# Performance work log

Hardware: AMD Instinct MI355X
Metric: run time of the kernel (lower is better)

Reference implementation:

```python
import jax, jax.numpy as jnp
import numpy as np

WS = 8                       # window size (square)
N = WS * WS                  # tokens per window
RES_H, RES_W = 32, 32        # input_resolution
DIM = 512
NUM_HEADS = 16
HEAD_DIM = DIM // NUM_HEADS
SCALE = HEAD_DIM ** -0.5
TABLE = 2 * WS - 1           # size of a_p/b_p/a_r/b_r tables
B_ = 1024                    # num_windows * batch


def _rel_coords():
    c = np.arange(WS)
    coords = np.stack(np.meshgrid(c, c, indexing='ij'))          # (2, WS, WS)
    cf = coords.reshape(2, -1)                                   # (2, N)
    rel = cf[:, :, None] - cf[:, None, :]                        # (2, N, N), values in [-(WS-1), WS-1]
    return rel[0], rel[1]                                        # radius (dh), azimuth (dw)

RADIUS_NP, AZIMUTH_NP = _rel_coords()
# torch indexes the (2*WS-1)-row tables with negative indices -> python wrap: -k maps to TABLE-k
IDX_R = jnp.asarray(RADIUS_NP % TABLE)
IDX_AZ = jnp.asarray(AZIMUTH_NP % TABLE)
RADIUS = jnp.asarray(RADIUS_NP, dtype=jnp.float32)               # (N, N)
AZIMUTH = jnp.asarray(AZIMUTH_NP, dtype=jnp.float32)             # (N, N)


def setup_inputs() -> dict:
    key = jax.random.key(0)
    ks = jax.random.split(key, 10)
    return {
        'x': jax.random.normal(ks[0], (B_, N, DIM), dtype=jnp.float32),
        'theta_max': jnp.ones((), dtype=jnp.float32) * 1.5708,   # ~pi/2 field-of-view half-angle
        'qkv_w': jax.random.normal(ks[1], (3 * DIM, DIM), dtype=jnp.float32) * 0.02,
        'qkv_b': jnp.zeros((3 * DIM,), dtype=jnp.float32),
        'proj_w': jax.random.normal(ks[2], (DIM, DIM), dtype=jnp.float32) * 0.02,
        'proj_b': jnp.zeros((DIM,), dtype=jnp.float32),
        'a_p': jax.random.normal(ks[3], (TABLE, NUM_HEADS), dtype=jnp.float32) * 0.02,
        'b_p': jax.random.normal(ks[4], (TABLE, NUM_HEADS), dtype=jnp.float32) * 0.02,
        'a_r': jax.random.normal(ks[5], (TABLE, NUM_HEADS), dtype=jnp.float32) * 0.02,
        'b_r': jax.random.normal(ks[6], (TABLE, NUM_HEADS), dtype=jnp.float32) * 0.02,
    }


def _trig_bias(table_a, table_b, idx, angle):
    # table_[ab]: (TABLE, H); idx: (N, N) int; angle: (N, N) float (possibly traced)
    a = table_a[idx]                                              # (N, N, H)
    b = table_b[idx]
    ang = angle[:, :, None]                                       # (N, N, 1)
    bias = a * jnp.cos(ang) + b * jnp.sin(ang)                    # (N, N, H)
    return jnp.transpose(bias, (2, 0, 1))                         # (H, N, N)


def reference(x, theta_max, qkv_w, qkv_b, proj_w, proj_b, a_p, b_p, a_r, b_r):
    Bw, n, c = x.shape
    qkv = x @ qkv_w.T + qkv_b                                     # (B_, N, 3*DIM)
    qkv = qkv.reshape(Bw, n, 3, NUM_HEADS, HEAD_DIM)
    qkv = jnp.transpose(qkv, (2, 0, 3, 1, 4))                     # (3, B_, H, N, hd)
    q, k, v = qkv[0] * SCALE, qkv[1], qkv[2]

    attn = jnp.einsum('bhid,bhjd->bhij', q, k)                    # (B_, H, N, N)

    az_angle = AZIMUTH * (2.0 * np.pi / RES_W)                    # (N, N)
    A_phi = _trig_bias(a_p, b_p, IDX_AZ, az_angle)                # (H, N, N)
    r_angle = RADIUS * (theta_max / RES_H)                        # (N, N), traced via theta_max
    A_theta = _trig_bias(a_r, b_r, IDX_R, r_angle)                # (H, N, N)

    attn = attn + A_phi[None] + A_theta[None]
    attn = jax.nn.softmax(attn, axis=-1)

    out = jnp.einsum('bhij,bhjd->bhid', attn, v)                  # (B_, H, N, hd)
    out = jnp.transpose(out, (0, 2, 1, 3)).reshape(Bw, n, c)      # (B_, N, DIM)
    out = out @ proj_w.T + proj_b
    return out
```

## Files before the change

kernel.cpp:

```cpp
#include <hip/hip_runtime.h>
#include <hip/hip_bf16.h>


typedef __bf16 bf16_t;
typedef bf16_t bf16x4 __attribute__((ext_vector_type(4)));
typedef bf16_t bf16x8 __attribute__((ext_vector_type(8)));
typedef float  f32x4  __attribute__((ext_vector_type(4)));

#define NWIN   1024
#define NTOK   64
#define DIM    512
#define NHEADS 16
#define HD     32
#define MTOT   (NWIN*NTOK)
#define QKVN   (3*DIM)
#define SCLG2E 0.25503494f

__device__ __forceinline__ void async_copy16(const void* g, void* lds_generic) {
    __builtin_amdgcn_global_load_lds(
        (__attribute__((address_space(1))) unsigned int*)(unsigned long long)g,
        (__attribute__((address_space(3))) unsigned int*)(unsigned int)(unsigned long long)lds_generic,
        16, 0, 0);
}

__global__ void cvt_f32_bf16(const float* __restrict__ in, bf16_t* __restrict__ out, int n8) {
    int i = blockIdx.x * blockDim.x + threadIdx.x;
    if (i >= n8) return;
    const float4* p = (const float4*)in;
    float4 a = p[2*i], b = p[2*i+1];
    bf16x8 o;
    o[0]=(bf16_t)a.x; o[1]=(bf16_t)a.y; o[2]=(bf16_t)a.z; o[3]=(bf16_t)a.w;
    o[4]=(bf16_t)b.x; o[5]=(bf16_t)b.y; o[6]=(bf16_t)b.z; o[7]=(bf16_t)b.w;
    ((bf16x8*)out)[i] = o;
}

__global__ void bias_kernel(const float* __restrict__ ap, const float* __restrict__ bp,
                            const float* __restrict__ ar, const float* __restrict__ br,
                            const float* __restrict__ theta_max, float* __restrict__ bias) {
    int idx = blockIdx.x * 256 + threadIdx.x;
    int h  = idx >> 12;
    int ij = idx & 4095;
    int i = ij >> 6, j = ij & 63;
    int ri = i >> 3, ci = i & 7, rj = j >> 3, cj = j & 7;
    int rad = ri - rj, az = ci - cj;
    int idx_r  = rad < 0 ? rad + 15 : rad;
    int idx_az = az  < 0 ? az  + 15 : az;
    float azang = (float)az * 0.19634954084936207f;
    float rang  = (float)rad * (theta_max[0] * (1.0f/32.0f));
    float v = ap[idx_az*NHEADS + h] * cosf(azang) + bp[idx_az*NHEADS + h] * sinf(azang)
            + ar[idx_r *NHEADS + h] * cosf(rang)  + br[idx_r *NHEADS + h] * sinf(rang);
    bias[idx] = v * 1.4426950408889634f;
}

template<int OUT_BF16>
__global__ __launch_bounds__(256, 2)
void gemm_bt(const bf16_t* __restrict__ A, const bf16_t* __restrict__ Bt,
             const float* __restrict__ bias, void* __restrict__ C,
             int M, int N, int K, int ntiles) {
    __shared__ bf16_t sA[128*64];
    __shared__ bf16_t sB[128*64];

    int bid = blockIdx.x;
    int bm = bid / ntiles, bn = bid % ntiles;
    int tid = threadIdx.x;
    int w = tid >> 6, lane = tid & 63;
    int quad = lane >> 4, l16 = lane & 15;
    int wm = w >> 1, wn = w & 1;

    f32x4 acc[4][4] = {};

    const bf16_t* Abase = A  + (size_t)(bm*128) * K;
    const bf16_t* Bbase = Bt + (size_t)(bn*128) * K;

    for (int k0 = 0; k0 < K; k0 += 64) {
        for (int i = 0; i < 4; ++i) {
            int off = w*4096 + i*1024 + lane*16;
            int r  = off >> 7;
            int pb = (off >> 4) & 7;
            int cb = pb ^ (r & 7);
            async_copy16(Abase + (size_t)r*K + k0 + cb*8, (char*)sA + w*4096 + i*1024);
            async_copy16(Bbase + (size_t)r*K + k0 + cb*8, (char*)sB + w*4096 + i*1024);
        }
        __syncthreads();

        for (int kk = 0; kk < 64; kk += 32) {
            bf16x8 af[4], bf[4];
            for (int mi = 0; mi < 4; ++mi) {
                int r  = wm*64 + mi*16 + l16;
                int cb = (kk >> 3) + quad;
                int pb = cb ^ (r & 7);
                af[mi] = *(const bf16x8*)((const char*)sA + r*128 + pb*16);
            }
            for (int ni = 0; ni < 4; ++ni) {
                int r  = wn*64 + ni*16 + l16;
                int cb = (kk >> 3) + quad;
                int pb = cb ^ (r & 7);
                bf[ni] = *(const bf16x8*)((const char*)sB + r*128 + pb*16);
            }
            for (int mi = 0; mi < 4; ++mi)
                for (int ni = 0; ni < 4; ++ni)
                    acc[mi][ni] = __builtin_amdgcn_mfma_f32_16x16x32_bf16(
                        af[mi], bf[ni], acc[mi][ni], 0, 0, 0);
        }
        __syncthreads();
    }

    for (int ni = 0; ni < 4; ++ni) {
        int col = bn*128 + wn*64 + ni*16 + l16;
        float bv = bias[col];
        for (int mi = 0; mi < 4; ++mi) {
            int row0 = bm*128 + wm*64 + mi*16 + quad*4;
            f32x4 a = acc[mi][ni];
            for (int reg = 0; reg < 4; ++reg) {
                float v = a[reg] + bv;
                size_t o = (size_t)(row0 + reg) * N + col;
                if (OUT_BF16) ((bf16_t*)C)[o] = (bf16_t)v;
                else          ((float*)C)[o]  = v;
            }
        }
    }
}

__global__ __launch_bounds__(256, 2)
void attn_proj_kernel(const bf16_t* __restrict__ qkv, const float* __restrict__ bias,
                      const bf16_t* __restrict__ projw, const float* __restrict__ projb,
                      float* __restrict__ out) {
    __shared__ bf16_t aout[32768];
    __shared__ bf16_t pbuf[4][2048];

    int b = blockIdx.x;
    int tid = threadIdx.x;
    int w = tid >> 6, lane = tid & 63, quad = lane >> 4, l16 = lane & 15;
    int qh = quad >> 1, ql = quad & 1;
    const bf16_t* base = qkv + (size_t)(b*64) * QKVN;
    f32x4 zero = {0.f, 0.f, 0.f, 0.f};
    bf16_t* pb = pbuf[w];

    auto LOADH = [&](int h, bf16x8* ak, bf16x8* bq, bf16x8* av) {
        #pragma unroll
        for (int jt = 0; jt < 4; ++jt)
            ak[jt] = *(const bf16x8*)(base + (size_t)(jt*16 + l16)*QKVN + 512 + h*32 + quad*8);
        #pragma unroll
        for (int it = 0; it < 4; ++it)
            bq[it] = *(const bf16x8*)(base + (size_t)(it*16 + l16)*QKVN + h*32 + quad*8);
        #pragma unroll
        for (int dt = 0; dt < 2; ++dt)
            #pragma unroll
            for (int ks = 0; ks < 2; ++ks) {
                const bf16_t* vb = base + (size_t)(ks*32 + quad*8)*QKVN + 1024 + h*32 + dt*16 + l16;
                bf16x8 tmp;
                #pragma unroll
                for (int e = 0; e < 8; ++e) tmp[e] = vb[(size_t)e*QKVN];
                av[dt*2+ks] = tmp;
            }
    };

    auto DOHEAD = [&](int h, bf16x8* ak, bf16x8* bq, bf16x8* av) {
        const float* bh = bias + h*4096;
        f32x4 accO[2][4];
        float s[4];
        #pragma unroll
        for (int it = 0; it < 4; ++it) { s[it] = 0.f; accO[0][it] = zero; accO[1][it] = zero; }

        #pragma unroll
        for (int ks = 0; ks < 2; ++ks) {
            f32x4 bb[2][4];
            #pragma unroll
            for (int jh = 0; jh < 2; ++jh)
                #pragma unroll
                for (int it = 0; it < 4; ++it)
                    bb[jh][it] = *(const f32x4*)(bh + (it*16 + l16)*64 + (ks*2+jh)*16 + quad*4);

            f32x4 st[2][4];
            #pragma unroll
            for (int jh = 0; jh < 2; ++jh)
                #pragma unroll
                for (int it = 0; it < 4; ++it)
                    st[jh][it] = __builtin_amdgcn_mfma_f32_16x16x32_bf16(ak[ks*2+jh], bq[it], zero, 0, 0, 0);

            #pragma unroll
            for (int it = 0; it < 4; ++it)
                #pragma unroll
                for (int jh = 0; jh < 2; ++jh) {
                    float e0 = __builtin_amdgcn_exp2f(st[jh][it][0]*SCLG2E + bb[jh][it][0]);
                    float e1 = __builtin_amdgcn_exp2f(st[jh][it][1]*SCLG2E + bb[jh][it][1]);
                    float e2 = __builtin_amdgcn_exp2f(st[jh][it][2]*SCLG2E + bb[jh][it][2]);
                    float e3 = __builtin_amdgcn_exp2f(st[jh][it][3]*SCLG2E + bb[jh][it][3]);
                    s[it] += (e0 + e1) + (e2 + e3);
                    bf16x4 pk4;
                    pk4[0] = (bf16_t)e0; pk4[1] = (bf16_t)e1;
                    pk4[2] = (bf16_t)e2; pk4[3] = (bf16_t)e3;
                    *(bf16x4*)(pb + it*512 + (2*jh + qh)*128 + l16*8 + ql*4) = pk4;
                }

            #pragma unroll
            for (int it = 0; it < 4; ++it) {
                bf16x8 bp = ((const bf16x8*)(pb + it*512))[lane];
                accO[0][it] = __builtin_amdgcn_mfma_f32_16x16x32_bf16(av[0*2+ks], bp, accO[0][it], 0, 0, 0);
                accO[1][it] = __builtin_amdgcn_mfma_f32_16x16x32_bf16(av[1*2+ks], bp, accO[1][it], 0, 0, 0);
            }
        }

        #pragma unroll
        for (int it = 0; it < 4; ++it) {
            float sv = s[it];
            sv += __shfl_xor(sv, 16);
            sv += __shfl_xor(sv, 32);
            float inv = __builtin_amdgcn_rcpf(sv);
            #pragma unroll
            for (int dt = 0; dt < 2; ++dt) {
                bf16x4 o4;
                #pragma unroll
                for (int r = 0; r < 4; ++r) o4[r] = (bf16_t)(accO[dt][it][r] * inv);
                *(bf16x4*)(aout + (it*16 + h)*512 + (2*dt + qh)*128 + l16*8 + ql*4) = o4;
            }
        }
    };

    bf16x8 akA[4], bqA[4], avA[4], akB[4], bqB[4], avB[4];
    int h0 = w*4;
    LOADH(h0+0, akA, bqA, avA);
    LOADH(h0+1, akB, bqB, avB);
    DOHEAD(h0+0, akA, bqA, avA);
    LOADH(h0+2, akA, bqA, avA);
    DOHEAD(h0+1, akB, bqB, avB);
    LOADH(h0+3, akB, bqB, avB);
    DOHEAD(h0+2, akA, bqA, avA);
    DOHEAD(h0+3, akB, bqB, avB);

    __syncthreads();

    #pragma unroll 1
    for (int half = 0; half < 2; ++half) {
        f32x4 acc[4][4] = {};
        const bf16_t* wb = projw + (size_t)(w*128 + half*64 + l16)*512 + quad*8;

        bf16x8 af0[4], bw0[4], af1[4], bw1[4];
        auto LD = [&](bf16x8* af, bf16x8* bw, int hk) {
            #pragma unroll
            for (int mi = 0; mi < 4; ++mi)
                af[mi] = ((const bf16x8*)(aout + (mi*16 + hk)*512))[lane];
            #pragma unroll
            for (int ni = 0; ni < 4; ++ni)
                bw[ni] = *(const bf16x8*)(wb + (size_t)(ni*16)*512 + hk*32);
        };
        auto MM = [&](bf16x8* af, bf16x8* bw) {
            #pragma unroll
            for (int mi = 0; mi < 4; ++mi)
                #pragma unroll
                for (int ni = 0; ni < 4; ++ni)
                    acc[mi][ni] = __builtin_amdgcn_mfma_f32_16x16x32_bf16(af[mi], bw[ni], acc[mi][ni], 0, 0, 0);
        };

        LD(af0, bw0, 0);
        #pragma unroll 1
        for (int hk = 0; hk < 16; hk += 2) {
            LD(af1, bw1, hk+1);
            MM(af0, bw0);
            if (hk + 2 < 16) LD(af0, bw0, hk+2);
            MM(af1, bw1);
        }

        #pragma unroll
        for (int ni = 0; ni < 4; ++ni) {
            int col = w*128 + half*64 + ni*16 + l16;
            float bv = projb[col];
            #pragma unroll
            for (int mi = 0; mi < 4; ++mi) {
                int row0 = b*64 + mi*16 + quad*4;
                f32x4 a = acc[mi][ni];
                #pragma unroll
                for (int reg = 0; reg < 4; ++reg)
                    out[(size_t)(row0 + reg)*DIM + col] = a[reg] + bv;
            }
        }
    }
}

extern "C" void kernel_launch(void* const* d_in, const int* in_sizes, int n_in,
                              void* d_out, int out_size, void* d_ws, size_t ws_size,
                              hipStream_t stream) {
    const float* x      = (const float*)d_in[0];
    const float* theta  = (const float*)d_in[1];
    const float* qkv_w  = (const float*)d_in[2];
    const float* qkv_b  = (const float*)d_in[3];
    const float* proj_w = (const float*)d_in[4];
    const float* proj_b = (const float*)d_in[5];
    const float* a_p    = (const float*)d_in[6];
    const float* b_p    = (const float*)d_in[7];
    const float* a_r    = (const float*)d_in[8];
    const float* b_r    = (const float*)d_in[9];
    float* out = (float*)d_out;

    char* ws = (char*)d_ws;
    bf16_t* qkvbuf = (bf16_t*)ws;
    bf16_t* xb     = (bf16_t*)(ws + 201326592);
    bf16_t* wqkv   = (bf16_t*)(ws + 201326592 + 67108864);
    bf16_t* wproj  = (bf16_t*)(ws + 201326592 + 67108864 + 1572864);
    float*  biasbf = (float*) (ws + 201326592 + 67108864 + 1572864 + 524288);

    cvt_f32_bf16<<<(MTOT*DIM/8)/256, 256, 0, stream>>>(x, xb, MTOT*DIM/8);
    cvt_f32_bf16<<<(QKVN*DIM/8)/256, 256, 0, stream>>>(qkv_w, wqkv, QKVN*DIM/8);
    cvt_f32_bf16<<<(DIM*DIM/8)/256, 256, 0, stream>>>(proj_w, wproj, DIM*DIM/8);

    bias_kernel<<<256, 256, 0, stream>>>(a_p, b_p, a_r, b_r, theta, biasbf);

    gemm_bt<1><<<(MTOT/128)*(QKVN/128), 256, 0, stream>>>(xb, wqkv, qkv_b, qkvbuf,
                                                          MTOT, QKVN, DIM, QKVN/128);
    attn_proj_kernel<<<NWIN, 256, 0, stream>>>(qkvbuf, biasbf, wproj, proj_b, out);
}
```

Before: 517.0 us.

## Split fused attention+projection into attention kernel and separate projection GEMM

The output projection is pulled out of the attention kernel. Attention now writes bf16 per-head outputs to a global buffer (reusing the x bf16 buffer), and the existing tiled gemm_bt kernel computes the projection. The attention kernel drops its 64KB LDS staging buffer, processes heads in a simple loop without software double-buffering, and raises launch bounds to 4 blocks per CU for higher occupancy. The cost is an extra global write and read of a 64MB intermediate plus one more kernel launch.

```diff
diff --git a/kernel.cpp b/kernel.cpp
--- a/kernel.cpp
+++ b/kernel.cpp
@@ -121,11 +121,9 @@
     }
 }
 
-__global__ __launch_bounds__(256, 2)
-void attn_proj_kernel(const bf16_t* __restrict__ qkv, const float* __restrict__ bias,
-                      const bf16_t* __restrict__ projw, const float* __restrict__ projb,
-                      float* __restrict__ out) {
-    __shared__ bf16_t aout[32768];
+__global__ __launch_bounds__(256, 4)
+void attn_kernel(const bf16_t* __restrict__ qkv, const float* __restrict__ bias,
+                 bf16_t* __restrict__ obuf) {
     __shared__ bf16_t pbuf[4][2048];
 
     int b = blockIdx.x;
@@ -136,13 +134,19 @@
     f32x4 zero = {0.f, 0.f, 0.f, 0.f};
     bf16_t* pb = pbuf[w];
 
-    auto LOADH = [&](int h, bf16x8* ak, bf16x8* bq, bf16x8* av) {
+    #pragma unroll 1
+    for (int t = 0; t < 4; ++t) {
+        int h = w*4 + t;
+
+        bf16x8 ak[4], bq[4];
         #pragma unroll
         for (int jt = 0; jt < 4; ++jt)
             ak[jt] = *(const bf16x8*)(base + (size_t)(jt*16 + l16)*QKVN + 512 + h*32 + quad*8);
         #pragma unroll
         for (int it = 0; it < 4; ++it)
             bq[it] = *(const bf16x8*)(base + (size_t)(it*16 + l16)*QKVN + h*32 + quad*8);
+
+        bf16x8 av[2][2];
         #pragma unroll
         for (int dt = 0; dt < 2; ++dt)
             #pragma unroll
@@ -151,11 +155,9 @@
                 bf16x8 tmp;
                 #pragma unroll
                 for (int e = 0; e < 8; ++e) tmp[e] = vb[(size_t)e*QKVN];
-                av[dt*2+ks] = tmp;
-            }
-    };
-
-    auto DOHEAD = [&](int h, bf16x8* ak, bf16x8* bq, bf16x8* av) {
+                av[dt][ks] = tmp;
+            }
+
         const float* bh = bias + h*4096;
         f32x4 accO[2][4];
         float s[4];
@@ -196,8 +198,8 @@
             #pragma unroll
             for (int it = 0; it < 4; ++it) {
                 bf16x8 bp = ((const bf16x8*)(pb + it*512))[lane];
-                accO[0][it] = __builtin_amdgcn_mfma_f32_16x16x32_bf16(av[0*2+ks], bp, accO[0][it], 0, 0, 0);
-                accO[1][it] = __builtin_amdgcn_mfma_f32_16x16x32_bf16(av[1*2+ks], bp, accO[1][it], 0, 0, 0);
+                accO[0][it] = __builtin_amdgcn_mfma_f32_16x16x32_bf16(av[0][ks], bp, accO[0][it], 0, 0, 0);
+                accO[1][it] = __builtin_amdgcn_mfma_f32_16x16x32_bf16(av[1][ks], bp, accO[1][it], 0, 0, 0);
             }
         }
 
@@ -212,66 +214,7 @@
                 bf16x4 o4;
                 #pragma unroll
                 for (int r = 0; r < 4; ++r) o4[r] = (bf16_t)(accO[dt][it][r] * inv);
-                *(bf16x4*)(aout + (it*16 + h)*512 + (2*dt + qh)*128 + l16*8 + ql*4) = o4;
-            }
-        }
-    };
-
-    bf16x8 akA[4], bqA[4], avA[4], akB[4], bqB[4], avB[4];
-    int h0 = w*4;
-    LOADH(h0+0, akA, bqA, avA);
-    LOADH(h0+1, akB, bqB, avB);
-    DOHEAD(h0+0, akA, bqA, avA);
-    LOADH(h0+2, akA, bqA, avA);
-    DOHEAD(h0+1, akB, bqB, avB);
-    LOADH(h0+3, akB, bqB, avB);
-    DOHEAD(h0+2, akA, bqA, avA);
-    DOHEAD(h0+3, akB, bqB, avB);
-
-    __syncthreads();
-
-    #pragma unroll 1
-    for (int half = 0; half < 2; ++half) {
-        f32x4 acc[4][4] = {};
-        const bf16_t* wb = projw + (size_t)(w*128 + half*64 + l16)*512 + quad*8;
-
-        bf16x8 af0[4], bw0[4], af1[4], bw1[4];
-        auto LD = [&](bf16x8* af, bf16x8* bw, int hk) {
-            #pragma unroll
-            for (int mi = 0; mi < 4; ++mi)
-                af[mi] = ((const bf16x8*)(aout + (mi*16 + hk)*512))[lane];
-            #pragma unroll
-            for (int ni = 0; ni < 4; ++ni)
-                bw[ni] = *(const bf16x8*)(wb + (size_t)(ni*16)*512 + hk*32);
-        };
-        auto MM = [&](bf16x8* af, bf16x8* bw) {
-            #pragma unroll
-            for (int mi = 0; mi < 4; ++mi)
-                #pragma unroll
-                for (int ni = 0; ni < 4; ++ni)
-                    acc[mi][ni] = __builtin_amdgcn_mfma_f32_16x16x32_bf16(af[mi], bw[ni], acc[mi][ni], 0, 0, 0);
-        };
-
-        LD(af0, bw0, 0);
-        #pragma unroll 1
-        for (int hk = 0; hk < 16; hk += 2) {
-            LD(af1, bw1, hk+1);
-            MM(af0, bw0);
-            if (hk + 2 < 16) LD(af0, bw0, hk+2);
-            MM(af1, bw1);
-        }
-
-        #pragma unroll
-        for (int ni = 0; ni < 4; ++ni) {
-            int col = w*128 + half*64 + ni*16 + l16;
-            float bv = projb[col];
-            #pragma unroll
-            for (int mi = 0; mi < 4; ++mi) {
-                int row0 = b*64 + mi*16 + quad*4;
-                f32x4 a = acc[mi][ni];
-                #pragma unroll
-                for (int reg = 0; reg < 4; ++reg)
-                    out[(size_t)(row0 + reg)*DIM + col] = a[reg] + bv;
+                *(bf16x4*)(obuf + (size_t)(b*64 + it*16 + l16)*DIM + h*32 + dt*16 + quad*4) = o4;
             }
         }
     }
@@ -298,6 +241,7 @@
     bf16_t* wqkv   = (bf16_t*)(ws + 201326592 + 67108864);
     bf16_t* wproj  = (bf16_t*)(ws + 201326592 + 67108864 + 1572864);
     float*  biasbf = (float*) (ws + 201326592 + 67108864 + 1572864 + 524288);
+    bf16_t* obuf   = xb;
 
     cvt_f32_bf16<<<(MTOT*DIM/8)/256, 256, 0, stream>>>(x, xb, MTOT*DIM/8);
     cvt_f32_bf16<<<(QKVN*DIM/8)/256, 256, 0, stream>>>(qkv_w, wqkv, QKVN*DIM/8);
@@ -307,5 +251,8 @@
 
     gemm_bt<1><<<(MTOT/128)*(QKVN/128), 256, 0, stream>>>(xb, wqkv, qkv_b, qkvbuf,
                                                           MTOT, QKVN, DIM, QKVN/128);
-    attn_proj_kernel<<<NWIN, 256, 0, stream>>>(qkvbuf, biasbf, wproj, proj_b, out);
-}
+    attn_kernel<<<NWIN, 256, 0, stream>>>(qkvbuf, biasbf, obuf);
+
+    gemm_bt<0><<<(MTOT/128)*(DIM/128), 256, 0, stream>>>(obuf, wproj, proj_b, out,
+                                                         MTOT, DIM, DIM, DIM/128);
+}
```

Result: slower. 535.2 us (+3.5%).
